# Optimization experiments

Hardware: AMD Instinct MI355X
Metric: run time of the kernel (lower is better)

The kernel has to match this reference:

```python
import jax, jax.numpy as jnp
import numpy as np

S = 1024; VOCAB = 100000; EMB = 300
POS_SZ = 64; CHAR_E = 50; CHAR_ENC = 128; WLEN = 16
NCHARS = 100; NPOSTAG = 50; NPOSITIONS = 1024
D = EMB + 3 * POS_SZ + CHAR_ENC  # word_rep_size = 620
BIH = 128   # per-direction LSTM hidden (bilstm_hidden_size // 2)
TLH = 256; LCC = 128; GCC = 256
NET = 8; NTAGS = 16; NREL = 16
TOKF = 2 * BIH + LCC + TLH       # 640
SENTF = 2 * TOKF + GCC           # 1536

def _p(k, shape):
    return 0.02 * jax.random.normal(k, shape, dtype=jnp.float32)

def setup_inputs():
    key = jax.random.key(0)
    ks = jax.random.split(key, 30)
    return {
        'word_inputs': jax.random.randint(ks[0], (1, S), 0, VOCAB),
        'char_inputs': jax.random.randint(ks[1], (1, S, WLEN), 0, NCHARS),
        'postag_inputs': jax.random.randint(ks[2], (1, S), 0, NPOSTAG),
        'dependency_inputs': jax.random.randint(ks[3], (1, S), 0, 64),
        'position_inputs': jax.random.randint(ks[4], (1, S), 0, NPOSITIONS),
        'topo_order': jnp.arange(S),  # children-before-parents order
        'parent': jnp.concatenate([jnp.arange(1, S), jnp.array([S])]),  # chain dep tree; root -> dummy slot S
        'pointed_token_idx': 5,
        'word_table': _p(ks[5], (VOCAB, EMB)),
        'char_table': _p(ks[6], (NCHARS, CHAR_E)),
        'char_conv_w': _p(ks[7], (CHAR_ENC, CHAR_E, 3)),
        'char_conv_b': jnp.zeros((CHAR_ENC,), jnp.float32),
        'postag_table': _p(ks[8], (NPOSTAG, POS_SZ)),
        'position_table': _p(ks[9], (NPOSITIONS, POS_SZ)),
        'lstm_f_Wx': _p(ks[10], (D, 4 * BIH)),
        'lstm_f_Wh': _p(ks[11], (BIH, 4 * BIH)),
        'lstm_f_b': jnp.zeros((4 * BIH,), jnp.float32),
        'lstm_b_Wx': _p(ks[12], (D, 4 * BIH)),
        'lstm_b_Wh': _p(ks[13], (BIH, 4 * BIH)),
        'lstm_b_b': jnp.zeros((4 * BIH,), jnp.float32),
        'word_cnn_w': _p(ks[14], (LCC, D, 3)),
        'word_cnn_b': jnp.zeros((LCC,), jnp.float32),
        'tl_Wiou': _p(ks[15], (D, 3 * TLH)),
        'tl_Uiou': _p(ks[16], (TLH, 3 * TLH)),
        'tl_biou': jnp.zeros((3 * TLH,), jnp.float32),
        'tl_Wf': _p(ks[17], (D, TLH)),
        'tl_Uf': _p(ks[18], (TLH, TLH)),
        'tl_bf': jnp.zeros((TLH,), jnp.float32),
        'sent_cnn_w': _p(ks[19], (GCC, D, 3)),
        'sent_cnn_b': jnp.zeros((GCC,), jnp.float32),
        'et_w': _p(ks[20], (GCC + TOKF, NET)),
        'et_b': jnp.zeros((NET,), jnp.float32),
        'crf_w': _p(ks[21], (SENTF, NTAGS)),
        'crf_b': jnp.zeros((NTAGS,), jnp.float32),
        'crf_trans': _p(ks[22], (NTAGS, NTAGS)),
        'rel_w': _p(ks[23], (SENTF, NREL)),
        'rel_b': jnp.zeros((NREL,), jnp.float32),
    }

def _conv1d(x, w, b):
    # x: [N, Cin, W], w: [Cout, Cin, K], padding=1 (matches nn.Conv1d(..., padding=1))
    y = jax.lax.conv_general_dilated(x, w, (1,), [(1, 1)], dimension_numbers=('NCW', 'OIW', 'NCW'))
    return y + b[None, :, None]

def _lstm(xs, Wx, Wh, b):
    H = Wh.shape[0]
    def step(carry, x):
        h, c = carry
        g = x @ Wx + h @ Wh + b
        i, f, gg, o = jnp.split(g, 4, axis=-1)
        c = jax.nn.sigmoid(f) * c + jax.nn.sigmoid(i) * jnp.tanh(gg)
        h = jax.nn.sigmoid(o) * jnp.tanh(c)
        return (h, c), h
    init = (jnp.zeros((H,), xs.dtype), jnp.zeros((H,), xs.dtype))
    _, hs = jax.lax.scan(step, init, xs)
    return hs

def _tree_lstm(x, order, parent, Wiou, Uiou, biou, Wf, Uf, bf):
    # ChildSum TreeLSTM over the whole dependency tree in topological order.
    # Equivalent to the source's per-token subtree recursion: each node's h
    # only depends on its subtree.
    Sn, H = x.shape[0], Uf.shape[0]
    xiou = x @ Wiou + biou                 # [S, 3H]
    xf = jnp.concatenate([x @ Wf + bf, jnp.zeros((1, H), x.dtype)], axis=0)  # dummy row for root's parent
    def step(carry, j):
        h, hsum, fcsum = carry
        iou = xiou[j] + hsum[j] @ Uiou
        i, o, u = jnp.split(iou, 3)
        cj = jax.nn.sigmoid(i) * jnp.tanh(u) + fcsum[j]
        hj = jax.nn.sigmoid(o) * jnp.tanh(cj)
        p = parent[j]
        f = jax.nn.sigmoid(xf[p] + hj @ Uf)  # per-child forget gate
        return (h.at[j].set(hj), hsum.at[p].add(hj), fcsum.at[p].add(f * cj)), None
    h0 = jnp.zeros((Sn, H), x.dtype)
    acc0 = jnp.zeros((Sn + 1, H), x.dtype)
    (h, _, _), _ = jax.lax.scan(step, (h0, acc0, acc0), order)
    return h

def _viterbi(emissions, trans):
    # emissions: [S, T]; trans[i, j] = score(i -> j)
    def step(score, e):
        s = score[:, None] + trans
        return jnp.max(s, axis=0) + e, jnp.argmax(s, axis=0)
    final, ptrs = jax.lax.scan(step, emissions[0], emissions[1:])
    last = jnp.argmax(final)
    def bt(tag, p):
        prev = p[tag]
        return prev, prev
    _, prevs = jax.lax.scan(bt, last, ptrs, reverse=True)
    return jnp.concatenate([prevs, last[None]])

def reference(word_inputs, char_inputs, postag_inputs, dependency_inputs, position_inputs, topo_order, parent, pointed_token_idx, word_table, char_table, char_conv_w, char_conv_b, postag_table, position_table, lstm_f_Wx, lstm_f_Wh, lstm_f_b, lstm_b_Wx, lstm_b_Wh, lstm_b_b, word_cnn_w, word_cnn_b, tl_Wiou, tl_Uiou, tl_biou, tl_Wf, tl_Uf, tl_bf, sent_cnn_w, sent_cnn_b, et_w, et_b, crf_w, crf_b, crf_trans, rel_w, rel_b):
    we = word_table[word_inputs]                                   # [1,S,EMB]
    cx = jnp.transpose(char_table[char_inputs[0]], (0, 2, 1))      # [S,CHAR_E,WLEN]
    ce = jnp.max(jax.nn.relu(_conv1d(cx, char_conv_w, char_conv_b)), axis=-1)[None]  # CharCNN -> [1,S,CHAR_ENC]
    pe = postag_table[postag_inputs]
    poe = position_table[position_inputs]
    de = position_table[dependency_inputs]                         # faithful to source bug: uses position table
    inputs = jnp.concatenate([we, ce, pe, poe, de], axis=-1)       # [1,S,D]
    x = inputs[0]
    hf = _lstm(x, lstm_f_Wx, lstm_f_Wh, lstm_f_b)
    hb = _lstm(x[::-1], lstm_b_Wx, lstm_b_Wh, lstm_b_b)[::-1]
    bilstm = jnp.concatenate([hf, hb], axis=-1)[None]              # [1,S,2*BIH]
    xc = jnp.transpose(inputs, (0, 2, 1))                          # [1,D,S]
    local_cnn = jnp.transpose(_conv1d(xc, word_cnn_w, word_cnn_b), (0, 2, 1))
    tree_h = _tree_lstm(x, topo_order, parent, tl_Wiou, tl_Uiou, tl_biou, tl_Wf, tl_Uf, tl_bf)[None]
    global_cnn = jnp.transpose(jnp.max(_conv1d(xc, sent_cnn_w, sent_cnn_b), axis=-1, keepdims=True), (0, 2, 1))  # [1,1,GCC]
    tokens_info = jnp.concatenate([bilstm, local_cnn, tree_h], axis=-1)  # [1,S,TOKF]
    ptr = tokens_info[:, pointed_token_idx, :]                     # [1,TOKF]
    ptr_info = jnp.broadcast_to(ptr[:, None, :], (1, S, TOKF))
    glob_info = jnp.broadcast_to(global_cnn, (1, S, GCC))
    sentence_encoding = jnp.concatenate([tokens_info, ptr_info, glob_info], axis=-1)  # dropout = identity (eval)
    one_vec = jnp.concatenate([global_cnn[:, 0, :], ptr], axis=-1)
    entitytype = jax.nn.softmax(one_vec @ et_w + et_b, axis=-1)
    entities = _viterbi(sentence_encoding[0] @ crf_w + crf_b, crf_trans)
    relations = jax.nn.sigmoid(sentence_encoding @ rel_w + rel_b)
    return sentence_encoding, entitytype, entities, relations
```

## Files before the change

kernel.cpp:

```cpp
#include <hip/hip_runtime.h>
#include <math.h>

#define SEQ   1024
#define DX    620
#define BIH   128
#define TLH   256
#define NTAGS 16

#define O_X      0
#define O_XGF    634880
#define O_XGB    (O_XGF + 524288)
#define O_XIOU   (O_XGB + 524288)
#define O_XF     (O_XIOU + 786432)
#define O_LCNN   (O_XF + 262400)
#define O_SCNN   (O_LCNN + 131072)
#define O_PART   (O_SCNN + 262144)
#define O_GCNN   (O_PART + 4096)
#define O_HF     (O_GCNN + 256)
#define O_HB     (O_HF + 131072)
#define O_TREEH  (O_HB + 131072)
#define O_IOUA   (O_TREEH + 262144)
#define O_FCSUM  (O_IOUA + 787200)
#define O_EMIS   (O_FCSUM + 262400)

#define SENT 0xFFFFFFFFu

__device__ __forceinline__ float sig_f(float x){ return 1.0f/(1.0f + __expf(-x)); }
__device__ __forceinline__ float tanh_f(float x){
  float ax = fabsf(x);
  float e  = __expf(-2.0f*ax);
  float t  = (1.0f - e)/(1.0f + e);
  return x < 0.0f ? -t : t;
}

__global__ __launch_bounds__(128) void k_embed(
    const int* __restrict__ wi, const int* __restrict__ ci,
    const int* __restrict__ postag_in, const int* __restrict__ dep_in, const int* __restrict__ pos_in,
    const float* __restrict__ word_table, const float* __restrict__ char_table,
    const float* __restrict__ ccw, const float* __restrict__ ccb,
    const float* __restrict__ postag_table, const float* __restrict__ position_table,
    float* __restrict__ x)
{
  int s = blockIdx.x;
  int tid = threadIdx.x;
  __shared__ __align__(16) float ce[50][16];
  for (int idx = tid; idx < 800; idx += 128){
    int e = idx >> 4, t = idx & 15;
    ce[e][t] = char_table[ci[s*16 + t]*50 + e];
  }
  __syncthreads();
  float* xr = x + (size_t)s*DX;
  const float* wrow = word_table + (size_t)wi[s]*300;
  for (int d = tid; d < 300; d += 128) xr[d] = wrow[d];
  {
    int oc = tid;
    const float* wp = ccw + oc*150;
    float acc[16];
    float b = ccb[oc];
    #pragma unroll
    for (int t=0;t<16;t++) acc[t] = b;
    for (int ic=0; ic<50; ic++){
      float w0 = wp[ic*3+0], w1 = wp[ic*3+1], w2 = wp[ic*3+2];
      float cv[16];
      float4 c0 = *(const float4*)&ce[ic][0];
      float4 c1 = *(const float4*)&ce[ic][4];
      float4 c2 = *(const float4*)&ce[ic][8];
      float4 c3 = *(const float4*)&ce[ic][12];
      cv[0]=c0.x;cv[1]=c0.y;cv[2]=c0.z;cv[3]=c0.w;
      cv[4]=c1.x;cv[5]=c1.y;cv[6]=c1.z;cv[7]=c1.w;
      cv[8]=c2.x;cv[9]=c2.y;cv[10]=c2.z;cv[11]=c2.w;
      cv[12]=c3.x;cv[13]=c3.y;cv[14]=c3.z;cv[15]=c3.w;
      #pragma unroll
      for (int t=0;t<16;t++){
        float a = cv[t]*w1;
        if (t > 0)  a += cv[t-1]*w0;
        if (t < 15) a += cv[t+1]*w2;
        acc[t] += a;
      }
    }
    float m = acc[0];
    #pragma unroll
    for (int t=1;t<16;t++) m = fmaxf(m, acc[t]);
    xr[300 + oc] = fmaxf(m, 0.0f);
  }
  if (tid < 64){
    int d = tid;
    xr[428 + d] = postag_table[postag_in[s]*64 + d];
    xr[492 + d] = position_table[pos_in[s]*64 + d];
    xr[556 + d] = position_table[dep_in[s]*64 + d];
  }
}

struct GemmArgs {
  const float* B[6];
  const float* bias[6];
  float*       C[6];
  int N[6]; int K[6]; int amode[6];
};

__global__ __launch_bounds__(256) void k_gemm(const float* __restrict__ x, GemmArgs ga)
{
  int z = blockIdx.z;
  int N = ga.N[z], K = ga.K[z], amode = ga.amode[z];
  int bn = blockIdx.x*64;
  if (bn >= N) return;
  int bm = blockIdx.y*64;
  const float* __restrict__ Bm = ga.B[z];
  __shared__ __align__(16) float As[20][64];
  __shared__ __align__(16) float Bs[20][64];
  int tid = threadIdx.x;
  int lane = tid & 63, kg = tid >> 6;
  int tx = tid & 15, ty = tid >> 4;
  float acc[4][4] = {{0.f}};
  for (int k0 = 0; k0 < K; k0 += 20){
    #pragma unroll
    for (int kk=0; kk<5; kk++){
      int k = kg*5 + kk;
      float av;
      if (amode == 0){
        av = x[(size_t)(bm+lane)*DX + k0 + k];
      } else {
        int kc = k0 + k;
        int d  = kc/3;
        int sh = kc - d*3 - 1;
        int row = bm + lane + sh;
        av = (row >= 0 && row < SEQ) ? x[(size_t)row*DX + d] : 0.0f;
      }
      As[k][lane] = av;
      Bs[k][lane] = (amode==0) ? Bm[(size_t)(k0+k)*N + bn + lane]
                               : Bm[(size_t)(bn+lane)*K + k0 + k];
    }
    __syncthreads();
    #pragma unroll
    for (int k=0;k<20;k++){
      float4 a = *(const float4*)&As[k][ty<<2];
      float4 b = *(const float4*)&Bs[k][tx<<2];
      acc[0][0]+=a.x*b.x; acc[0][1]+=a.x*b.y; acc[0][2]+=a.x*b.z; acc[0][3]+=a.x*b.w;
      acc[1][0]+=a.y*b.x; acc[1][1]+=a.y*b.y; acc[1][2]+=a.y*b.z; acc[1][3]+=a.y*b.w;
      acc[2][0]+=a.z*b.x; acc[2][1]+=a.z*b.y; acc[2][2]+=a.z*b.z; acc[2][3]+=a.z*b.w;
      acc[3][0]+=a.w*b.x; acc[3][1]+=a.w*b.y; acc[3][2]+=a.w*b.z; acc[3][3]+=a.w*b.w;
    }
    __syncthreads();
  }
  const float* bias = ga.bias[z];
  float* C = ga.C[z];
  float4 bb;
  bb.x = bias[bn+(tx<<2)+0]; bb.y = bias[bn+(tx<<2)+1];
  bb.z = bias[bn+(tx<<2)+2]; bb.w = bias[bn+(tx<<2)+3];
  #pragma unroll
  for (int i=0;i<4;i++){
    int row = bm + (ty<<2) + i;
    float4 o;
    o.x = acc[i][0] + bb.x; o.y = acc[i][1] + bb.y;
    o.z = acc[i][2] + bb.z; o.w = acc[i][3] + bb.w;
    *(float4*)&C[(size_t)row*N + bn + (tx<<2)] = o;
  }
}

__global__ __launch_bounds__(256) void k_gmax(const float* __restrict__ scnn, float* __restrict__ gcnn){
  int c = threadIdx.x;
  float m = -3.0e38f;
  #pragma unroll 8
  for (int s = 0; s < SEQ; s++) m = fmaxf(m, scnn[(size_t)s*256 + c]);
  gcnn[c] = m;
}

__global__ __launch_bounds__(512, 2) void k_recur(
    const float* __restrict__ xg_f, const float* __restrict__ xg_b,
    const float* __restrict__ Wh_f, const float* __restrict__ Wh_b,
    const float* __restrict__ xiou, const float* __restrict__ xf,
    const float* __restrict__ Uiou, const float* __restrict__ Uf,
    const int* __restrict__ order, const int* __restrict__ parent,
    float* __restrict__ hf, float* __restrict__ hb,
    float* tree_h, float* iou_acc, float* fcsum)
{
  int blk = blockIdx.x;
  int tid = threadIdx.x;

  if (blk >= 4){
    const float* xg  = (blk == 4) ? xg_f : xg_b;
    const float* Wh  = (blk == 4) ? Wh_f : Wh_b;
    float* hout      = (blk == 4) ? hf : hb;
    int col = tid;
    float4 w4[32];
    #pragma unroll
    for (int r=0;r<32;r++){
      w4[r].x = Wh[(size_t)(r*4+0)*512 + col];
      w4[r].y = Wh[(size_t)(r*4+1)*512 + col];
      w4[r].z = Wh[(size_t)(r*4+2)*512 + col];
      w4[r].w = Wh[(size_t)(r*4+3)*512 + col];
    }
    #pragma unroll
    for (int r=0;r<32;r++)
      asm volatile("" : "+v"(w4[r].x), "+v"(w4[r].y), "+v"(w4[r].z), "+v"(w4[r].w));
    __shared__ __align__(16) float lhl[BIH];
    __shared__ float lcst[BIH];
    __shared__ float gl[512];
    if (tid < BIH){ lhl[tid] = 0.f; lcst[tid] = 0.f; }
    __syncthreads();
    const float4* lhl4 = (const float4*)lhl;
    for (int st=0; st<SEQ; st++){
      int n = (blk == 4) ? st : (SEQ-1-st);
      float a = xg[(size_t)n*512 + col];
      #pragma unroll
      for (int r=0;r<32;r++){
        float4 h4 = lhl4[r];
        a += h4.x*w4[r].x + h4.y*w4[r].y + h4.z*w4[r].z + h4.w*w4[r].w;
      }
      gl[col] = a;
      __syncthreads();
      if (tid < BIH){
        float gi = gl[tid], gf = gl[BIH+tid], gg = gl[2*BIH+tid], go = gl[3*BIH+tid];
        float c = sig_f(gf)*lcst[tid] + sig_f(gi)*tanh_f(gg);
        float h = sig_f(go)*tanh_f(c);
        lcst[tid] = c;
        lhl[tid] = h;
        hout[(size_t)n*BIH + tid] = h;
      }
      __syncthreads();
    }
    return;
  }

  int colh = tid >> 1, half = tid & 1;
  int ulo = blk*64;
  float4 w4[32];
  {
    const float* Wsrc; size_t stride; int gcol;
    if (colh < 192){ Wsrc = Uiou; stride = 768; gcol = (colh>>6)*TLH + ulo + (colh&63); }
    else           { Wsrc = Uf;   stride = 256; gcol = ulo + (colh-192); }
    #pragma unroll
    for (int r=0;r<32;r++){
      int row = half*128 + r*4;
      w4[r].x = Wsrc[(size_t)(row+0)*stride + gcol];
      w4[r].y = Wsrc[(size_t)(row+1)*stride + gcol];
      w4[r].z = Wsrc[(size_t)(row+2)*stride + gcol];
      w4[r].w = Wsrc[(size_t)(row+3)*stride + gcol];
    }
  }
  #pragma unroll
  for (int r=0;r<32;r++)
    asm volatile("" : "+v"(w4[r].x), "+v"(w4[r].y), "+v"(w4[r].z), "+v"(w4[r].w));

  __shared__ __align__(16) float hl[TLH];
  __shared__ float colsum[TLH];
  __shared__ float cprev[64];
  __shared__ int ord_l[SEQ];
  __shared__ int par_l[SEQ];
  for (int i=tid; i<SEQ; i+=512){ ord_l[i] = order[i]; par_l[i] = parent[i]; }
  __syncthreads();
  const float4* hl4 = (const float4*)hl;

  for (int t=0; t<SEQ; t++){
    int n  = ord_l[t];
    int m  = (t > 0) ? ord_l[t-1] : 0;
    int pp = (t > 0) ? par_l[m] : -1;
    bool ppeq = (pp == n);

    float xi=0.f, xo=0.f, xu=0.f, ac_i=0.f, ac_o=0.f, ac_u=0.f, fcn=0.f;
    float xfv=0.f, po_i=0.f, po_o=0.f, po_u=0.f, po_f=0.f;
    if (tid < 64){
      int uu = ulo + tid;
      xi   = xiou[(size_t)n*768 + uu];
      xo   = xiou[(size_t)n*768 + 256 + uu];
      xu   = xiou[(size_t)n*768 + 512 + uu];
      ac_i = iou_acc[(size_t)n*768 + uu];
      ac_o = iou_acc[(size_t)n*768 + 256 + uu];
      ac_u = iou_acc[(size_t)n*768 + 512 + uu];
      fcn  = fcsum[(size_t)n*256 + uu];
      if (t > 0){
        xfv = xf[(size_t)pp*256 + uu];
        if (!ppeq){
          po_i = iou_acc[(size_t)pp*768 + uu];
          po_o = iou_acc[(size_t)pp*768 + 256 + uu];
          po_u = iou_acc[(size_t)pp*768 + 512 + uu];
          po_f = fcsum[(size_t)pp*256 + uu];
        }
      }
    }

    if (t > 0){
      float a = 0.f;
      #pragma unroll
      for (int r=0;r<32;r++){
        float4 h4 = hl4[half*32 + r];
        a += h4.x*w4[r].x + h4.y*w4[r].y + h4.z*w4[r].z + h4.w*w4[r].w;
      }
      a += __shfl_xor(a, 1);
      if (!half) colsum[colh] = a;
    }
    __syncthreads();

    if (tid < 64){
      int uu = ulo + tid;
      float ai = ac_i, ao = ac_o, au = ac_u, fcs = fcn;
      if (t > 0){
        float vi = colsum[tid], vo = colsum[64+tid], vuu = colsum[128+tid], vf = colsum[192+tid];
        float fg  = sig_f(xfv + vf);
        float fcc = fg * cprev[tid];
        if (ppeq){
          ai += vi; ao += vo; au += vuu; fcs += fcc;
        } else {
          iou_acc[(size_t)pp*768 + uu]       = po_i + vi;
          iou_acc[(size_t)pp*768 + 256 + uu] = po_o + vo;
          iou_acc[(size_t)pp*768 + 512 + uu] = po_u + vuu;
          fcsum[(size_t)pp*256 + uu]         = po_f + fcc;
        }
      }
      float cc = sig_f(xi + ai)*tanh_f(xu + au) + fcs;
      float hh = sig_f(xo + ao)*tanh_f(cc);
      cprev[tid] = cc;
      hl[uu] = hh;
      __hip_atomic_store(&tree_h[(size_t)n*TLH + uu], hh, __ATOMIC_RELAXED, __HIP_MEMORY_SCOPE_AGENT);
    } else if (tid >= 64 && tid < 112){
      int p  = tid - 64;
      int qi = (p < (ulo >> 2)) ? p : p + 16;
      const unsigned* tp = (const unsigned*)(tree_h + (size_t)n*TLH + qi*4);
      unsigned v0, v1, v2, v3;
      while (true){
        v0 = __hip_atomic_load(tp+0, __ATOMIC_RELAXED, __HIP_MEMORY_SCOPE_AGENT);
        v1 = __hip_atomic_load(tp+1, __ATOMIC_RELAXED, __HIP_MEMORY_SCOPE_AGENT);
        v2 = __hip_atomic_load(tp+2, __ATOMIC_RELAXED, __HIP_MEMORY_SCOPE_AGENT);
        v3 = __hip_atomic_load(tp+3, __ATOMIC_RELAXED, __HIP_MEMORY_SCOPE_AGENT);
        if ((v0 != SENT) & (v1 != SENT) & (v2 != SENT) & (v3 != SENT)) break;
      }
      float4 hv;
      hv.x = __uint_as_float(v0); hv.y = __uint_as_float(v1);
      hv.z = __uint_as_float(v2); hv.w = __uint_as_float(v3);
      *(float4*)&hl[qi*4] = hv;
    }
    __syncthreads();
  }
}

__global__ __launch_bounds__(256) void k_assemble(
    const float* __restrict__ hf, const float* __restrict__ hb,
    const float* __restrict__ lcnn, const float* __restrict__ tree_h,
    const float* __restrict__ gcnn,
    const float* __restrict__ crf_w, const float* __restrict__ crf_b,
    const float* __restrict__ rel_w, const float* __restrict__ rel_b,
    const int* __restrict__ ptk,
    float* __restrict__ se_out, float* __restrict__ emis, float* __restrict__ rel_out)
{
  int s = blockIdx.x, tid = threadIdx.x;
  int p = ptk[0];
  __shared__ float se[1536];
  for (int d = tid; d < 1536; d += 256){
    float v;
    if      (d < 128)  v = hf[(size_t)s*128 + d];
    else if (d < 256)  v = hb[(size_t)s*128 + d-128];
    else if (d < 384)  v = lcnn[(size_t)s*128 + d-256];
    else if (d < 640)  v = tree_h[(size_t)s*256 + d-384];
    else if (d < 768)  v = hf[(size_t)p*128 + d-640];
    else if (d < 896)  v = hb[(size_t)p*128 + d-768];
    else if (d < 1024) v = lcnn[(size_t)p*128 + d-896];
    else if (d < 1280) v = tree_h[(size_t)p*256 + d-1024];
    else               v = gcnn[d-1280];
    se[d] = v;
    se_out[(size_t)s*1536 + d] = v;
  }
  __syncthreads();
  int o = tid >> 3, l = tid & 7;
  const float* W = (o < 16) ? crf_w : rel_w;
  int oc = (o < 16) ? o : (o - 16);
  float a = 0.f;
  for (int k = l; k < 1536; k += 8) a += se[k]*W[(size_t)k*16 + oc];
  for (int off = 4; off; off >>= 1) a += __shfl_down(a, off, 8);
  if (l == 0){
    if (o < 16) emis[(size_t)s*16 + o] = a + crf_b[o];
    else        rel_out[(size_t)s*16 + oc] = sig_f(a + rel_b[oc]);
  }
}

__global__ __launch_bounds__(256) void k_entity(
    const float* __restrict__ hf, const float* __restrict__ hb,
    const float* __restrict__ lcnn, const float* __restrict__ tree_h,
    const float* __restrict__ gcnn,
    const float* __restrict__ et_w, const float* __restrict__ et_b,
    const int* __restrict__ ptk, float* __restrict__ out_et)
{
  __shared__ float ov[896];
  __shared__ float lg[8];
  int tid = threadIdx.x;
  int p = ptk[0];
  for (int d = tid; d < 896; d += 256){
    float v;
    if      (d < 256) v = gcnn[d];
    else if (d < 384) v = hf[(size_t)p*128 + d-256];
    else if (d < 512) v = hb[(size_t)p*128 + d-384];
    else if (d < 640) v = lcnn[(size_t)p*128 + d-512];
    else              v = tree_h[(size_t)p*256 + d-640];
    ov[d] = v;
  }
  __syncthreads();
  int o = tid >> 5, l = tid & 31;
  float a = 0.f;
  for (int k = l; k < 896; k += 32) a += ov[k]*et_w[(size_t)k*8 + o];
  for (int off = 16; off; off >>= 1) a += __shfl_down(a, off, 32);
  if (l == 0) lg[o] = a + et_b[o];
  __syncthreads();
  if (tid == 0){
    float mx = lg[0];
    for (int i=1;i<8;i++) mx = fmaxf(mx, lg[i]);
    float e[8], sum = 0.f;
    for (int i=0;i<8;i++){ e[i] = __expf(lg[i]-mx); sum += e[i]; }
    for (int i=0;i<8;i++) out_et[i] = e[i]/sum;
  }
}

__global__ __launch_bounds__(128) void k_viterbi(
    const float* __restrict__ emis, const float* __restrict__ trans, float* __restrict__ out_e)
{
  __shared__ float ring[64][16];
  __shared__ float sc[16], nsc[16];
  __shared__ float tr[256];
  __shared__ unsigned char ptrs[1023*16];
  int tid = threadIdx.x;
  for (int i=tid; i<256; i+=128) tr[i] = trans[i];
  for (int i=tid; i<33*16; i+=128) ring[i>>4][i&15] = emis[i];
  if (tid < 16) sc[tid] = emis[tid];
  __syncthreads();
  int j = (tid & 63) >> 2, iq = tid & 3;
  for (int t=1; t<1024; t++){
    if (tid >= 64){
      int lr = tid - 64;
      int tl = t + 32;
      if (lr < 16 && tl < 1024) ring[tl & 63][lr] = emis[(size_t)tl*16 + lr];
    } else {
      float best = -3.0e38f; int barg = 0;
      #pragma unroll
      for (int ii=0; ii<4; ii++){
        int i = iq*4 + ii;
        float v = sc[i] + tr[i*16 + j];
        if (v > best){ best = v; barg = i; }
      }
      #pragma unroll
      for (int off=1; off<4; off<<=1){
        float ovv = __shfl_down(best, off, 4);
        int   oaa = __shfl_down(barg, off, 4);
        if (ovv > best){ best = ovv; barg = oaa; }
      }
      if (iq == 0){
        nsc[j] = best + ring[t & 63][j];
        ptrs[(t-1)*16 + j] = (unsigned char)barg;
      }
    }
    __syncthreads();
    if (tid < 16) sc[tid] = nsc[tid];
    __syncthreads();
  }
  if (tid == 0){
    float b = sc[0]; int last = 0;
    #pragma unroll
    for (int i=1;i<16;i++){ if (sc[i] > b){ b = sc[i]; last = i; } }
    out_e[1023] = (float)last;
    int cur = last;
    for (int t=1022; t>=0; t--){ cur = (int)ptrs[t*16 + cur]; out_e[t] = (float)cur; }
  }
}

extern "C" void kernel_launch(void* const* d_in, const int* in_sizes, int n_in,
                              void* d_out, int out_size, void* d_ws, size_t ws_size,
                              hipStream_t stream)
{
  (void)in_sizes; (void)n_in; (void)out_size; (void)ws_size;
  const int*   wi         = (const int*)d_in[0];
  const int*   ci         = (const int*)d_in[1];
  const int*   postag_in  = (const int*)d_in[2];
  const int*   dep_in     = (const int*)d_in[3];
  const int*   pos_in     = (const int*)d_in[4];
  const int*   order      = (const int*)d_in[5];
  const int*   parent     = (const int*)d_in[6];
  const int*   ptk        = (const int*)d_in[7];
  const float* word_table = (const float*)d_in[8];
  const float* char_table = (const float*)d_in[9];
  const float* ccw        = (const float*)d_in[10];
  const float* ccb        = (const float*)d_in[11];
  const float* postag_tab = (const float*)d_in[12];
  const float* pos_tab    = (const float*)d_in[13];
  const float* Wx_f       = (const float*)d_in[14];
  const float* Wh_f       = (const float*)d_in[15];
  const float* b_f        = (const float*)d_in[16];
  const float* Wx_b       = (const float*)d_in[17];
  const float* Wh_b       = (const float*)d_in[18];
  const float* b_b        = (const float*)d_in[19];
  const float* wcnn_w     = (const float*)d_in[20];
  const float* wcnn_b     = (const float*)d_in[21];
  const float* Wiou       = (const float*)d_in[22];
  const float* Uiou       = (const float*)d_in[23];
  const float* biou       = (const float*)d_in[24];
  const float* Wf_t       = (const float*)d_in[25];
  const float* Uf_t       = (const float*)d_in[26];
  const float* bf_t       = (const float*)d_in[27];
  const float* scnn_w     = (const float*)d_in[28];
  const float* scnn_b     = (const float*)d_in[29];
  const float* et_w       = (const float*)d_in[30];
  const float* et_b       = (const float*)d_in[31];
  const float* crf_w      = (const float*)d_in[32];
  const float* crf_b      = (const float*)d_in[33];
  const float* crf_trans  = (const float*)d_in[34];
  const float* rel_w      = (const float*)d_in[35];
  const float* rel_b      = (const float*)d_in[36];

  float* ws = (float*)d_ws;
  float* x      = ws + O_X;
  float* xg_f   = ws + O_XGF;
  float* xg_b   = ws + O_XGB;
  float* xiou   = ws + O_XIOU;
  float* xf     = ws + O_XF;
  float* lcnn   = ws + O_LCNN;
  float* scnn   = ws + O_SCNN;
  float* gcnn   = ws + O_GCNN;
  float* hf     = ws + O_HF;
  float* hb     = ws + O_HB;
  float* tree_h = ws + O_TREEH;
  float* iou_acc= ws + O_IOUA;
  float* fcsum  = ws + O_FCSUM;
  float* emis   = ws + O_EMIS;

  float* outF     = (float*)d_out;
  float* se_out   = outF;
  float* et_out   = outF + 1572864;
  float* ent_out  = outF + 1572872;
  float* rel_out  = outF + 1573896;

  hipMemsetAsync(xf, 0, (size_t)1025*256*sizeof(float), stream);
  hipMemsetAsync(iou_acc, 0, ((size_t)1025*768 + 1025*256)*sizeof(float), stream);
  hipMemsetAsync(tree_h, 0xFF, (size_t)1024*256*sizeof(float), stream);

  k_embed<<<SEQ, 128, 0, stream>>>(wi, ci, postag_in, dep_in, pos_in,
                                   word_table, char_table, ccw, ccb,
                                   postag_tab, pos_tab, x);

  GemmArgs ga;
  ga.B[0]=Wx_f;  ga.bias[0]=b_f;   ga.C[0]=xg_f; ga.N[0]=512; ga.K[0]=620;  ga.amode[0]=0;
  ga.B[1]=Wx_b;  ga.bias[1]=b_b;   ga.C[1]=xg_b; ga.N[1]=512; ga.K[1]=620;  ga.amode[1]=0;
  ga.B[2]=Wiou;  ga.bias[2]=biou;  ga.C[2]=xiou; ga.N[2]=768; ga.K[2]=620;  ga.amode[2]=0;
  ga.B[3]=Wf_t;  ga.bias[3]=bf_t;  ga.C[3]=xf;   ga.N[3]=256; ga.K[3]=620;  ga.amode[3]=0;
  ga.B[4]=wcnn_w;ga.bias[4]=wcnn_b;ga.C[4]=lcnn; ga.N[4]=128; ga.K[4]=1860; ga.amode[4]=1;
  ga.B[5]=scnn_w;ga.bias[5]=scnn_b;ga.C[5]=scnn; ga.N[5]=256; ga.K[5]=1860; ga.amode[5]=1;
  k_gemm<<<dim3(12,16,6), 256, 0, stream>>>(x, ga);

  k_gmax<<<1, 256, 0, stream>>>(scnn, gcnn);

  k_recur<<<6, 512, 0, stream>>>(xg_f, xg_b, Wh_f, Wh_b, xiou, xf, Uiou, Uf_t,
                                 order, parent, hf, hb, tree_h, iou_acc, fcsum);

  k_assemble<<<SEQ, 256, 0, stream>>>(hf, hb, lcnn, tree_h, gcnn,
                                      crf_w, crf_b, rel_w, rel_b, ptk,
                                      se_out, emis, rel_out);

  k_entity<<<1, 256, 0, stream>>>(hf, hb, lcnn, tree_h, gcnn, et_w, et_b, ptk, et_out);

  k_viterbi<<<1, 128, 0, stream>>>(emis, crf_trans, ent_out);
}
```

Measured before the change: 3.084 ms.

## Shrink recurrent kernel to 256 threads with multi-column register tiles

The recurrent kernel drops from 512 to 256 threads per block. Each thread now holds weights for 4 or 8 output columns across a slice of rows, and partial sums are combined with cross-lane shuffle reductions. The hidden-state buffer in shared memory uses an XOR-swizzled slot layout to avoid bank conflicts. Cross-block tree-hidden exchange now uses inline-asm system-coherent stores and vector polling loads with an atomic fallback. The aim is to cut per-step barrier and LDS cost on the serial critical path, at the cost of more registers per thread and more shuffle steps.

After: 3.279 ms. 6.3% more time.

```diff
diff --git a/kernel.cpp b/kernel.cpp
--- a/kernel.cpp
+++ b/kernel.cpp
@@ -25,6 +25,8 @@
 
 #define SENT 0xFFFFFFFFu
 
+typedef float f32x4_t __attribute__((ext_vector_type(4)));
+
 __device__ __forceinline__ float sig_f(float x){ return 1.0f/(1.0f + __expf(-x)); }
 __device__ __forceinline__ float tanh_f(float x){
   float ax = fabsf(x);
@@ -32,6 +34,7 @@
   float t  = (1.0f - e)/(1.0f + e);
   return x < 0.0f ? -t : t;
 }
+__device__ __forceinline__ int physslot(int s){ return s ^ ((s>>3)&7); }
 
 __global__ __launch_bounds__(128) void k_embed(
     const int* __restrict__ wi, const int* __restrict__ ci,
@@ -165,7 +168,7 @@
   gcnn[c] = m;
 }
 
-__global__ __launch_bounds__(512, 2) void k_recur(
+__global__ __launch_bounds__(256, 1) void k_recur(
     const float* __restrict__ xg_f, const float* __restrict__ xg_b,
     const float* __restrict__ Wh_f, const float* __restrict__ Wh_b,
     const float* __restrict__ xiou, const float* __restrict__ xf,
@@ -181,18 +184,26 @@
     const float* xg  = (blk == 4) ? xg_f : xg_b;
     const float* Wh  = (blk == 4) ? Wh_f : Wh_b;
     float* hout      = (blk == 4) ? hf : hb;
-    int col = tid;
-    float4 w4[32];
-    #pragma unroll
-    for (int r=0;r<32;r++){
-      w4[r].x = Wh[(size_t)(r*4+0)*512 + col];
-      w4[r].y = Wh[(size_t)(r*4+1)*512 + col];
-      w4[r].z = Wh[(size_t)(r*4+2)*512 + col];
-      w4[r].w = Wh[(size_t)(r*4+3)*512 + col];
-    }
-    #pragma unroll
-    for (int r=0;r<32;r++)
-      asm volatile("" : "+v"(w4[r].x), "+v"(w4[r].y), "+v"(w4[r].z), "+v"(w4[r].w));
+    int cg = tid >> 1, rg = tid & 1;
+    float4 w[4][16];
+    #pragma unroll
+    for (int cc=0;cc<4;cc++){
+      int col = cg*4 + cc;
+      #pragma unroll
+      for (int r4=0;r4<16;r4++){
+        int row = rg*64 + r4*4;
+        w[cc][r4].x = Wh[(size_t)(row+0)*512 + col];
+        w[cc][r4].y = Wh[(size_t)(row+1)*512 + col];
+        w[cc][r4].z = Wh[(size_t)(row+2)*512 + col];
+        w[cc][r4].w = Wh[(size_t)(row+3)*512 + col];
+      }
+    }
+    #pragma unroll
+    for (int cc=0;cc<4;cc++)
+      #pragma unroll
+      for (int r4=0;r4<16;r4++)
+        asm volatile("" : "+v"(w[cc][r4].x), "+v"(w[cc][r4].y), "+v"(w[cc][r4].z), "+v"(w[cc][r4].w));
+
     __shared__ __align__(16) float lhl[BIH];
     __shared__ float lcst[BIH];
     __shared__ float gl[512];
@@ -201,13 +212,22 @@
     const float4* lhl4 = (const float4*)lhl;
     for (int st=0; st<SEQ; st++){
       int n = (blk == 4) ? st : (SEQ-1-st);
-      float a = xg[(size_t)n*512 + col];
-      #pragma unroll
-      for (int r=0;r<32;r++){
-        float4 h4 = lhl4[r];
-        a += h4.x*w4[r].x + h4.y*w4[r].y + h4.z*w4[r].z + h4.w*w4[r].w;
-      }
-      gl[col] = a;
+      float4 xg4 = make_float4(0.f,0.f,0.f,0.f);
+      if (rg == 0) xg4 = *(const float4*)&xg[(size_t)n*512 + cg*4];
+      float acc[4] = {0.f,0.f,0.f,0.f};
+      #pragma unroll
+      for (int r4=0;r4<16;r4++){
+        float4 h4 = lhl4[rg*16 + r4];
+        #pragma unroll
+        for (int cc=0;cc<4;cc++)
+          acc[cc] += h4.x*w[cc][r4].x + h4.y*w[cc][r4].y + h4.z*w[cc][r4].z + h4.w*w[cc][r4].w;
+      }
+      #pragma unroll
+      for (int cc=0;cc<4;cc++) acc[cc] += __shfl_xor(acc[cc], 1);
+      if (rg == 0){
+        float4 o = make_float4(acc[0]+xg4.x, acc[1]+xg4.y, acc[2]+xg4.z, acc[3]+xg4.w);
+        *(float4*)&gl[cg*4] = o;
+      }
       __syncthreads();
       if (tid < BIH){
         float gi = gl[tid], gf = gl[BIH+tid], gg = gl[2*BIH+tid], go = gl[3*BIH+tid];
@@ -222,32 +242,36 @@
     return;
   }
 
-  int colh = tid >> 1, half = tid & 1;
+  int cg = tid >> 3, rg = tid & 7;
   int ulo = blk*64;
-  float4 w4[32];
-  {
+  float4 w[8][8];
+  #pragma unroll
+  for (int cc=0;cc<8;cc++){
+    int c = cg*8 + cc;
     const float* Wsrc; size_t stride; int gcol;
-    if (colh < 192){ Wsrc = Uiou; stride = 768; gcol = (colh>>6)*TLH + ulo + (colh&63); }
-    else           { Wsrc = Uf;   stride = 256; gcol = ulo + (colh-192); }
-    #pragma unroll
-    for (int r=0;r<32;r++){
-      int row = half*128 + r*4;
-      w4[r].x = Wsrc[(size_t)(row+0)*stride + gcol];
-      w4[r].y = Wsrc[(size_t)(row+1)*stride + gcol];
-      w4[r].z = Wsrc[(size_t)(row+2)*stride + gcol];
-      w4[r].w = Wsrc[(size_t)(row+3)*stride + gcol];
+    if (c < 192){ Wsrc = Uiou; stride = 768; gcol = (c>>6)*TLH + ulo + (c&63); }
+    else        { Wsrc = Uf;   stride = 256; gcol = ulo + (c-192); }
+    #pragma unroll
+    for (int r4=0;r4<8;r4++){
+      int row = rg*32 + r4*4;
+      w[cc][r4].x = Wsrc[(size_t)(row+0)*stride + gcol];
+      w[cc][r4].y = Wsrc[(size_t)(row+1)*stride + gcol];
+      w[cc][r4].z = Wsrc[(size_t)(row+2)*stride + gcol];
+      w[cc][r4].w = Wsrc[(size_t)(row+3)*stride + gcol];
     }
   }
   #pragma unroll
-  for (int r=0;r<32;r++)
-    asm volatile("" : "+v"(w4[r].x), "+v"(w4[r].y), "+v"(w4[r].z), "+v"(w4[r].w));
+  for (int cc=0;cc<8;cc++)
+    #pragma unroll
+    for (int r4=0;r4<8;r4++)
+      asm volatile("" : "+v"(w[cc][r4].x), "+v"(w[cc][r4].y), "+v"(w[cc][r4].z), "+v"(w[cc][r4].w));
 
   __shared__ __align__(16) float hl[TLH];
   __shared__ float colsum[TLH];
   __shared__ float cprev[64];
   __shared__ int ord_l[SEQ];
   __shared__ int par_l[SEQ];
-  for (int i=tid; i<SEQ; i+=512){ ord_l[i] = order[i]; par_l[i] = parent[i]; }
+  for (int i=tid; i<SEQ; i+=256){ ord_l[i] = order[i]; par_l[i] = parent[i]; }
   __syncthreads();
   const float4* hl4 = (const float4*)hl;
 
@@ -280,14 +304,25 @@
     }
 
     if (t > 0){
-      float a = 0.f;
-      #pragma unroll
-      for (int r=0;r<32;r++){
-        float4 h4 = hl4[half*32 + r];
-        a += h4.x*w4[r].x + h4.y*w4[r].y + h4.z*w4[r].z + h4.w*w4[r].w;
-      }
-      a += __shfl_xor(a, 1);
-      if (!half) colsum[colh] = a;
+      float acc[8] = {0.f,0.f,0.f,0.f,0.f,0.f,0.f,0.f};
+      int base = rg << 3;
+      #pragma unroll
+      for (int r4=0;r4<8;r4++){
+        float4 h4 = hl4[base + (r4 ^ rg)];
+        #pragma unroll
+        for (int cc=0;cc<8;cc++)
+          acc[cc] += h4.x*w[cc][r4].x + h4.y*w[cc][r4].y + h4.z*w[cc][r4].z + h4.w*w[cc][r4].w;
+      }
+      #pragma unroll
+      for (int cc=0;cc<8;cc++){
+        acc[cc] += __shfl_xor(acc[cc], 1);
+        acc[cc] += __shfl_xor(acc[cc], 2);
+        acc[cc] += __shfl_xor(acc[cc], 4);
+      }
+      if (rg == 0){
+        *(float4*)&colsum[cg*8]     = make_float4(acc[0], acc[1], acc[2], acc[3]);
+        *(float4*)&colsum[cg*8 + 4] = make_float4(acc[4], acc[5], acc[6], acc[7]);
+      }
     }
     __syncthreads();
 
@@ -310,24 +345,31 @@
       float cc = sig_f(xi + ai)*tanh_f(xu + au) + fcs;
       float hh = sig_f(xo + ao)*tanh_f(cc);
       cprev[tid] = cc;
-      hl[uu] = hh;
-      __hip_atomic_store(&tree_h[(size_t)n*TLH + uu], hh, __ATOMIC_RELAXED, __HIP_MEMORY_SCOPE_AGENT);
-    } else if (tid >= 64 && tid < 112){
+      int s = uu >> 2;
+      hl[physslot(s)*4 + (uu & 3)] = hh;
+      float* tp = &tree_h[(size_t)n*TLH + uu];
+      asm volatile("global_store_dword %0, %1, off sc0 sc1" :: "v"(tp), "v"(hh) : "memory");
+    } else if (tid < 112){
       int p  = tid - 64;
       int qi = (p < (ulo >> 2)) ? p : p + 16;
-      const unsigned* tp = (const unsigned*)(tree_h + (size_t)n*TLH + qi*4);
-      unsigned v0, v1, v2, v3;
+      const float* tp = tree_h + (size_t)n*TLH + qi*4;
+      const unsigned* up = (const unsigned*)tp;
+      union { f32x4_t v; float4 f; unsigned u[4]; } pol;
+      int spins = 0;
       while (true){
-        v0 = __hip_atomic_load(tp+0, __ATOMIC_RELAXED, __HIP_MEMORY_SCOPE_AGENT);
-        v1 = __hip_atomic_load(tp+1, __ATOMIC_RELAXED, __HIP_MEMORY_SCOPE_AGENT);
-        v2 = __hip_atomic_load(tp+2, __ATOMIC_RELAXED, __HIP_MEMORY_SCOPE_AGENT);
-        v3 = __hip_atomic_load(tp+3, __ATOMIC_RELAXED, __HIP_MEMORY_SCOPE_AGENT);
-        if ((v0 != SENT) & (v1 != SENT) & (v2 != SENT) & (v3 != SENT)) break;
-      }
-      float4 hv;
-      hv.x = __uint_as_float(v0); hv.y = __uint_as_float(v1);
-      hv.z = __uint_as_float(v2); hv.w = __uint_as_float(v3);
-      *(float4*)&hl[qi*4] = hv;
+        asm volatile("global_load_dwordx4 %0, %1, off sc0 sc1\n\ts_waitcnt vmcnt(0)"
+                     : "=v"(pol.v) : "v"(tp) : "memory");
+        if ((pol.u[0] != SENT) & (pol.u[1] != SENT) & (pol.u[2] != SENT) & (pol.u[3] != SENT)) break;
+        if (++spins > 64){
+          pol.u[0] = __hip_atomic_load(up+0, __ATOMIC_RELAXED, __HIP_MEMORY_SCOPE_AGENT);
+          pol.u[1] = __hip_atomic_load(up+1, __ATOMIC_RELAXED, __HIP_MEMORY_SCOPE_AGENT);
+          pol.u[2] = __hip_atomic_load(up+2, __ATOMIC_RELAXED, __HIP_MEMORY_SCOPE_AGENT);
+          pol.u[3] = __hip_atomic_load(up+3, __ATOMIC_RELAXED, __HIP_MEMORY_SCOPE_AGENT);
+          if ((pol.u[0] != SENT) & (pol.u[1] != SENT) & (pol.u[2] != SENT) & (pol.u[3] != SENT)) break;
+          spins = 0;
+        }
+      }
+      *(float4*)&hl[physslot(qi)*4] = pol.f;
     }
     __syncthreads();
   }
@@ -543,7 +585,7 @@
 
   k_gmax<<<1, 256, 0, stream>>>(scnn, gcnn);
 
-  k_recur<<<6, 512, 0, stream>>>(xg_f, xg_b, Wh_f, Wh_b, xiou, xf, Uiou, Uf_t,
+  k_recur<<<6, 256, 0, stream>>>(xg_f, xg_b, Wh_f, Wh_b, xiou, xf, Uiou, Uf_t,
                                  order, parent, hf, hb, tree_h, iou_acc, fcsum);
 
   k_assemble<<<SEQ, 256, 0, stream>>>(hf, hb, lcnn, tree_h, gcnn,
```
